# Performance work log

Measured on AMD Instinct MI355X. Metric: run time of the kernel, lower is better.

## Reference

```python
import jax, jax.numpy as jnp
import numpy as np

NUM_HEADS = 12
HEAD_SIZE = 64
HIDDEN = NUM_HEADS * HEAD_SIZE  # 768
ONE_SIDED_WINDOW = 256          # attention_window 512 // 2
NEG = -10000.0


def setup_inputs() -> dict:
    key = jax.random.key(0)
    ks = jax.random.split(key, 16)
    B, W, E, H = 1, 2048, 128, HIDDEN
    std = 0.02
    def lin(kw, kb):
        return (jax.random.normal(kw, (H, H), jnp.float32) * std,
                jax.random.normal(kb, (H,), jnp.float32) * std)
    q_w, q_b = lin(ks[0], ks[1])
    k_w, k_b = lin(ks[2], ks[3])
    v_w, v_b = lin(ks[4], ks[5])
    w2e_w, w2e_b = lin(ks[6], ks[7])
    e2w_w, e2w_b = lin(ks[8], ks[9])
    e2e_w, e2e_b = lin(ks[10], ks[11])
    return {
        "word_hidden_states": jax.random.normal(ks[12], (B, W, H), jnp.float32),
        "entity_hidden_states": jax.random.normal(ks[13], (B, E, H), jnp.float32),
        "attention_mask": jnp.zeros((B, 1, 1, W + E), jnp.float32),
        "q_w": q_w, "q_b": q_b, "k_w": k_w, "k_b": k_b, "v_w": v_w, "v_b": v_b,
        "w2e_w": w2e_w, "w2e_b": w2e_b, "e2w_w": e2w_w, "e2w_b": e2w_b,
        "e2e_w": e2e_w, "e2e_b": e2e_b,
    }


def reference(word_hidden_states, entity_hidden_states, attention_mask,
              q_w, q_b, k_w, k_b, v_w, v_b,
              w2e_w, w2e_b, e2w_w, e2w_b, e2e_w, e2e_b):
    B, W, H = word_hidden_states.shape
    E = entity_hidden_states.shape[1]
    S = W + E

    def heads(x):  # [B, L, H] -> [B, nh, L, hd]
        return x.reshape(B, -1, NUM_HEADS, HEAD_SIZE).transpose(0, 2, 1, 3)

    concat = jnp.concatenate([word_hidden_states, entity_hidden_states], axis=1)
    k = heads(concat @ k_w + k_b)          # [B, nh, S, hd]
    v = heads(concat @ v_w + v_b)
    q_w2w = heads(word_hidden_states @ q_w + q_b)
    q_w2e = heads(word_hidden_states @ w2e_w + w2e_b)
    q_e2w = heads(entity_hidden_states @ e2w_w + e2w_b)
    q_e2e = heads(entity_hidden_states @ e2e_w + e2e_b)

    k_word, k_ent = k[:, :, :W], k[:, :, W:]

    # --- w2w: Longformer sliding-window QK^T, then _conversion to a dense
    # [B, nh, W, W] matrix with out-of-band entries set to -10000. ---
    w2w = jnp.einsum('bhid,bhjd->bhij', q_w2w, k_word)  # [B, nh, W, W]
    idx = jnp.arange(W)
    in_band = jnp.abs(idx[:, None] - idx[None, :]) <= ONE_SIDED_WINDOW  # [W, W]
    # diagonal mask: float_mask[j] (-10000 where attention_mask != 0) added
    # within the band (broadcast over heads / query positions)
    mask_words = attention_mask[:, 0, 0, :W]                # [B, W]
    float_mask = jnp.where(mask_words != 0.0, NEG, 0.0)     # [B, W]
    w2w = w2w + float_mask[:, None, None, :]
    # _conversion: out-of-band -> -10000; also exact zeros -> -10000 (source quirk)
    w2w = jnp.where(in_band[None, None] & (w2w != 0.0), w2w, NEG)

    # --- entity-aware dense blocks ---
    w2e = jnp.einsum('bhid,bhjd->bhij', q_w2e, k_ent)    # [B, nh, W, E]
    e2w = jnp.einsum('bhid,bhjd->bhij', q_e2w, k_word)   # [B, nh, E, W]
    e2e = jnp.einsum('bhid,bhjd->bhij', q_e2e, k_ent)    # [B, nh, E, E]

    word_scores = jnp.concatenate([w2w, w2e], axis=3)    # [B, nh, W, S]
    ent_scores = jnp.concatenate([e2w, e2e], axis=3)     # [B, nh, E, S]
    scores = jnp.concatenate([word_scores, ent_scores], axis=2)  # [B, nh, S, S]

    scores = scores / jnp.sqrt(jnp.float32(HEAD_SIZE)) + attention_mask
    probs = jax.nn.softmax(scores, axis=-1)

    ctx = jnp.einsum('bhij,bhjd->bhid', probs, v)        # [B, nh, S, hd]
    ctx = ctx.transpose(0, 2, 1, 3).reshape(B, S, H)
    return ctx[:, :W, :], ctx[:, W:, :]
```

## Files before the change

### kernel.cpp

```cpp
#include <hip/hip_runtime.h>

typedef __bf16 bf16x8 __attribute__((ext_vector_type(8)));
typedef unsigned short u16x8 __attribute__((ext_vector_type(8)));
typedef u16x8 u16x8_a __attribute__((may_alias));
typedef unsigned int u32x2 __attribute__((ext_vector_type(2)));
typedef u32x2 u32x2_a __attribute__((may_alias));
typedef unsigned int u32x4 __attribute__((ext_vector_type(4)));
typedef u32x4 u32x4_a __attribute__((may_alias));
typedef float f32x4 __attribute__((ext_vector_type(4)));
typedef float f32x16 __attribute__((ext_vector_type(16)));

#define LOG2E 1.4426950408889634f
#define NEGV  -10000.0f

__device__ __forceinline__ unsigned int cvtpk(float lo, float hi){
  unsigned int r;
  asm("v_cvt_pk_bf16_f32 %0, %1, %2" : "=v"(r) : "v"(lo), "v"(hi));
  return r;
}
__device__ __forceinline__ bf16x8 ldb(const unsigned short* p){
  return __builtin_bit_cast(bf16x8, *(const u16x8_a*)p);
}
__device__ __forceinline__ bf16x8 mkfrag(unsigned a, unsigned b, unsigned c, unsigned d){
  u32x4 v = {a,b,c,d};
  return __builtin_bit_cast(bf16x8, v);
}
__device__ __forceinline__ void gload16(const unsigned short* g, unsigned short* l){
  __builtin_amdgcn_global_load_lds(
    (const __attribute__((address_space(1))) void*)g,
    (__attribute__((address_space(3))) void*)l, 16, 0, 0);
}

__global__ __launch_bounds__(256) void prep(
    const float* __restrict__ w0, const float* __restrict__ w1,
    const float* __restrict__ w2, const float* __restrict__ w3,
    const float* __restrict__ w4, const float* __restrict__ w5,
    const float* __restrict__ word, const float* __restrict__ ent,
    const float* __restrict__ am,
    unsigned short* __restrict__ outT, unsigned short* __restrict__ Abf,
    float* __restrict__ amT, float* __restrict__ negT)
{
  int z = blockIdx.z, tid = threadIdx.x;
  if (z == 6){
    size_t id = (size_t)blockIdx.y*24 + blockIdx.x;
    size_t e = (id*256 + tid)*8;
    const size_t WE = (size_t)2048*768;
    const float* s = (e < WE) ? (word + e) : (ent + (e - WE));
    float4 a = *(const float4*)s;
    float4 b = *(const float4*)(s+4);
    u32x4 v = {cvtpk(a.x,a.y), cvtpk(a.z,a.w), cvtpk(b.x,b.y), cvtpk(b.z,b.w)};
    *(u32x4_a*)(Abf + e) = v;
    return;
  }
  if (z == 7){
    if (blockIdx.y != 0 || blockIdx.x >= 9) return;
    int j = blockIdx.x*256 + tid;
    if (j < 2176){
      float a = am[j];
      amT[j]  = a * LOG2E;
      negT[j] = (a != 0.f) ? NEGV : 0.f;
    }
    return;
  }
  if (blockIdx.y >= 24) return;
  const float* src;
  switch (z){
    case 0: src = w0; break; case 1: src = w1; break; case 2: src = w2; break;
    case 3: src = w3; break; case 4: src = w4; break; default: src = w5; break;
  }
  unsigned short* dst = outT + (size_t)z * 589824;
  __shared__ float tile[32][33];
  int tx = tid & 31, ty = tid >> 5;
  int x0 = blockIdx.x*32, y0 = blockIdx.y*32;
  #pragma unroll
  for (int i=0;i<32;i+=8) tile[ty+i][tx] = src[(size_t)(y0+ty+i)*768 + x0+tx];
  __syncthreads();
  #pragma unroll
  for (int i=0;i<32;i+=16){
    unsigned int u = cvtpk(tile[tx][ty+i], tile[tx][ty+i+8]);
    dst[(size_t)(x0+ty+i)*768 + y0+tx]   = (unsigned short)u;
    dst[(size_t)(x0+ty+i+8)*768 + y0+tx] = (unsigned short)(u>>16);
  }
}

__global__ __launch_bounds__(256) void gemm_proj(
    const unsigned short* __restrict__ Abf,
    const unsigned short* __restrict__ wT,
    const float* __restrict__ bK, const float* __restrict__ bV,
    const float* __restrict__ bQ, const float* __restrict__ bWE,
    const float* __restrict__ bEW, const float* __restrict__ bEE,
    unsigned short* __restrict__ oK, unsigned short* __restrict__ VbT,
    unsigned short* __restrict__ oQ, unsigned short* __restrict__ oWE,
    unsigned short* __restrict__ oEW, unsigned short* __restrict__ oEE)
{
  int mt = blockIdx.x, ntile = blockIdx.y;
  int g, mg;
  if      (mt < 17){ g=0; mg=mt;    }
  else if (mt < 34){ g=1; mg=mt-17; }
  else if (mt < 50){ g=2; mg=mt-34; }
  else if (mt < 66){ g=3; mg=mt-50; }
  else if (mt < 67){ g=4; mg=0;     }
  else             { g=5; mg=0;     }
  int m0 = mg*128;
  const unsigned short* A = Abf + (size_t)((g>=4 ? 2048 : 0) + m0)*768;
  const unsigned short* B = wT + (size_t)g*589824;
  const float* bias; unsigned short* out;
  switch (g){
    case 0: bias=bK;  out=oK;  break;
    case 1: bias=bV;  out=0;   break;
    case 2: bias=bQ;  out=oQ;  break;
    case 3: bias=bWE; out=oWE; break;
    case 4: bias=bEW; out=oEW; break;
    default:bias=bEE; out=oEE; break;
  }
  int n0 = ntile*128;

  __shared__ __align__(16) unsigned short a_s[128*32];
  __shared__ __align__(16) unsigned short b_s[128*32];

  int tid  = threadIdx.x;
  int w    = tid>>6, lane = tid&63, quad = lane>>4, lr = lane&15;
  int wm   = (w&1)*64, wn = (w>>1)*64;

  f32x4 acc[4][4];
  #pragma unroll
  for (int i=0;i<4;i++) for (int j=0;j<4;j++) for (int r=0;r<4;r++) acc[i][j][r]=0.f;

  int srow = lane>>2;
  int scol = (lane&3)*8;
  const unsigned short* gA0 = A + (size_t)(w*32 + srow)*768 + scol;
  const unsigned short* gA1 = gA0 + (size_t)16*768;
  const unsigned short* gB0 = B + (size_t)(n0 + w*32 + srow)*768 + scol;
  const unsigned short* gB1 = gB0 + (size_t)16*768;
  unsigned short* lA0 = a_s + w*32*32;
  unsigned short* lA1 = lA0 + 16*32;
  unsigned short* lB0 = b_s + w*32*32;
  unsigned short* lB1 = lB0 + 16*32;

  for (int k0=0; k0<768; k0+=32){
    __syncthreads();
    gload16(gA0 + k0, lA0);
    gload16(gA1 + k0, lA1);
    gload16(gB0 + k0, lB0);
    gload16(gB1 + k0, lB1);
    __syncthreads();
    bf16x8 af[4], bfr[4];
    #pragma unroll
    for (int i=0;i<4;i++) af[i]  = ldb(a_s + (wm+i*16+lr)*32 + quad*8);
    #pragma unroll
    for (int j=0;j<4;j++) bfr[j] = ldb(b_s + (wn+j*16+lr)*32 + quad*8);
    #pragma unroll
    for (int i=0;i<4;i++)
      #pragma unroll
      for (int j=0;j<4;j++)
        acc[i][j] = __builtin_amdgcn_mfma_f32_16x16x32_bf16(af[i], bfr[j], acc[i][j], 0,0,0);
  }
  if (g == 1){
    #pragma unroll
    for (int j=0;j<4;j++){
      int col = n0 + wn + j*16 + lr;
      float bb = bias[col];
      #pragma unroll
      for (int i=0;i<4;i++){
        int rowb = m0 + wm + i*16 + quad*4;
        u32x2 uv = {cvtpk(acc[i][j][0]+bb, acc[i][j][1]+bb),
                    cvtpk(acc[i][j][2]+bb, acc[i][j][3]+bb)};
        *(u32x2_a*)(VbT + (size_t)col*2176 + rowb) = uv;
      }
    }
  } else {
    out += (size_t)m0*768;
    #pragma unroll
    for (int j=0;j<4;j++){
      int col = n0 + wn + j*16 + lr;
      float bb = bias[col];
      #pragma unroll
      for (int i=0;i<4;i++){
        int rowb = wm + i*16 + quad*4;
        unsigned int u01 = cvtpk(acc[i][j][0]+bb, acc[i][j][1]+bb);
        unsigned int u23 = cvtpk(acc[i][j][2]+bb, acc[i][j][3]+bb);
        out[(size_t)(rowb+0)*768 + col] = (unsigned short)u01;
        out[(size_t)(rowb+1)*768 + col] = (unsigned short)(u01>>16);
        out[(size_t)(rowb+2)*768 + col] = (unsigned short)u23;
        out[(size_t)(rowb+3)*768 + col] = (unsigned short)(u23>>16);
      }
    }
  }
}

__global__ __launch_bounds__(256) void attn_split(
  const unsigned short* __restrict__ Kb,  const unsigned short* __restrict__ VbT,
  const unsigned short* __restrict__ Qw,  const unsigned short* __restrict__ Qwe,
  const unsigned short* __restrict__ Qew, const unsigned short* __restrict__ Qee,
  const float* __restrict__ amT, const float* __restrict__ negT,
  float* __restrict__ outw, float* __restrict__ pO, float* __restrict__ pML)
{
  int lin = blockIdx.x + 80*blockIdx.y;
  int wid = (lin & 7)*120 + (lin >> 3);
  int bx = wid % 80;
  int h  = wid / 80;

  int tid = threadIdx.x, w = tid>>6, lane = tid&63;
  int l31 = lane & 31, hi = lane >> 5;
  int hi8 = hi*8, hi4 = hi*4;
  bool isword = bx < 64;
  int qrb, eg=0, eq=0;
  const unsigned short *Qa, *Qb;
  if (isword){ qrb = bx*32; Qa=Qw;  Qb=Qwe; }
  else       { int e = bx-64; eg = e>>2; eq = e&3; qrb = eg*32; Qa=Qew; Qb=Qee; }
  int hofs = h*64;

  __shared__ float part[4][64][35];

  float m = -1e30f, l = 0.f;
  f32x16 o0, o1;
  #pragma unroll
  for (int r=0;r<16;r++){ o0[r] = 0.f; o1[r] = 0.f; }

  int lo, b, s1, endT;
  if (isword){
    lo = qrb - 256; if (lo < 0) lo = 0;
    int hiq = qrb + 288; if (hiq > 2048) hiq = 2048;
    b = (hiq - lo) >> 5;
    s1 = w; endT = b + 4;
  } else {
    lo = 0; b = 64;
    s1 = eq*17 + w; endT = eq*17 + 17;
  }
  int e1 = (b < endT) ? b : endT;
  int c2 = s1 + ((e1 - s1 + 3) & ~3);
  int iq = qrb + l31;

#define BODY(J0, K0, K1, K2, K3, BAND) do { \
    int jb = (J0); \
    float4 aT0 = *(const float4*)(amT + jb + hi4); \
    float4 aT1 = *(const float4*)(amT + jb + 8  + hi4); \
    float4 aT2 = *(const float4*)(amT + jb + 16 + hi4); \
    float4 aT3 = *(const float4*)(amT + jb + 24 + hi4); \
    f32x16 s; \
    _Pragma("unroll") \
    for (int r=0;r<16;r++) s[r] = 0.f; \
    __builtin_amdgcn_s_setprio(1); \
    s = __builtin_amdgcn_mfma_f32_32x32x16_bf16(K0, qf0, s, 0,0,0); \
    s = __builtin_amdgcn_mfma_f32_32x32x16_bf16(K1, qf1, s, 0,0,0); \
    s = __builtin_amdgcn_mfma_f32_32x32x16_bf16(K2, qf2, s, 0,0,0); \
    s = __builtin_amdgcn_mfma_f32_32x32x16_bf16(K3, qf3, s, 0,0,0); \
    __builtin_amdgcn_s_setprio(0); \
    const unsigned short* vp = VbT + (size_t)(hofs + l31)*2176 + jb + hi8; \
    bf16x8 va00 = ldb(vp),           va01 = ldb(vp + 16); \
    bf16x8 va10 = ldb(vp + 32*2176), va11 = ldb(vp + 32*2176 + 16); \
    float sc[16]; \
    if (BAND){ \
      float4 nT0 = *(const float4*)(negT + jb + hi4); \
      float4 nT1 = *(const float4*)(negT + jb + 8  + hi4); \
      float4 nT2 = *(const float4*)(negT + jb + 16 + hi4); \
      float4 nT3 = *(const float4*)(negT + jb + 24 + hi4); \
      int djb = iq + 256 - (jb + hi4); \
      _Pragma("unroll") \
      for (int e=0;e<4;e++){ \
        { float sv = s[e]    + nT0[e]; \
          bool ok = ((unsigned)(djb - e)      <= 512u) && (sv != 0.f); \
          sc[e]    = (ok ? sv : NEGV) * (LOG2E*0.125f) + aT0[e]; } \
        { float sv = s[4+e]  + nT1[e]; \
          bool ok = ((unsigned)(djb - 8 - e)  <= 512u) && (sv != 0.f); \
          sc[4+e]  = (ok ? sv : NEGV) * (LOG2E*0.125f) + aT1[e]; } \
        { float sv = s[8+e]  + nT2[e]; \
          bool ok = ((unsigned)(djb - 16 - e) <= 512u) && (sv != 0.f); \
          sc[8+e]  = (ok ? sv : NEGV) * (LOG2E*0.125f) + aT2[e]; } \
        { float sv = s[12+e] + nT3[e]; \
          bool ok = ((unsigned)(djb - 24 - e) <= 512u) && (sv != 0.f); \
          sc[12+e] = (ok ? sv : NEGV) * (LOG2E*0.125f) + aT3[e]; } \
      } \
    } else { \
      _Pragma("unroll") \
      for (int e=0;e<4;e++){ \
        sc[e]    = s[e]    * (LOG2E*0.125f) + aT0[e]; \
        sc[4+e]  = s[4+e]  * (LOG2E*0.125f) + aT1[e]; \
        sc[8+e]  = s[8+e]  * (LOG2E*0.125f) + aT2[e]; \
        sc[12+e] = s[12+e] * (LOG2E*0.125f) + aT3[e]; \
      } \
    } \
    float mx = sc[0]; \
    _Pragma("unroll") \
    for (int r=1;r<16;r++) mx = fmaxf(mx, sc[r]); \
    mx = fmaxf(mx, __shfl_xor(mx, 32)); \
    float mn; \
    if (__all(mx <= m)){ \
      mn = m; \
    } else { \
      mn = fmaxf(m, mx); \
      float alpha = exp2f(m - mn); \
      m = mn; \
      l *= alpha; \
      _Pragma("unroll") \
      for (int r=0;r<16;r++){ o0[r] *= alpha; o1[r] *= alpha; } \
    } \
    float p[16]; \
    _Pragma("unroll") \
    for (int r=0;r<16;r++) p[r] = exp2f(sc[r]-mn); \
    float rs = ((p[0]+p[1])+(p[2]+p[3])) + ((p[4]+p[5])+(p[6]+p[7])) \
             + ((p[8]+p[9])+(p[10]+p[11])) + ((p[12]+p[13])+(p[14]+p[15])); \
    rs += __shfl_xor(rs, 32); \
    l += rs; \
    unsigned pk0 = cvtpk(p[0], p[1]),  pk1 = cvtpk(p[2], p[3]); \
    unsigned pk2 = cvtpk(p[4], p[5]),  pk3 = cvtpk(p[6], p[7]); \
    unsigned pk4 = cvtpk(p[8], p[9]),  pk5 = cvtpk(p[10], p[11]); \
    unsigned pk6 = cvtpk(p[12], p[13]),pk7 = cvtpk(p[14], p[15]); \
    bool hib = hi != 0; \
    unsigned t0 = hib ? pk0 : pk2; \
    unsigned t1 = hib ? pk1 : pk3; \
    unsigned t2 = hib ? pk4 : pk6; \
    unsigned t3 = hib ? pk5 : pk7; \
    unsigned r0 = (unsigned)__shfl_xor((int)t0, 32); \
    unsigned r1 = (unsigned)__shfl_xor((int)t1, 32); \
    unsigned r2 = (unsigned)__shfl_xor((int)t2, 32); \
    unsigned r3 = (unsigned)__shfl_xor((int)t3, 32); \
    bf16x8 pf1 = hib ? mkfrag(r0, r1, pk2, pk3) : mkfrag(pk0, pk1, r0, r1); \
    bf16x8 pf2 = hib ? mkfrag(r2, r3, pk6, pk7) : mkfrag(pk4, pk5, r2, r3); \
    __builtin_amdgcn_s_setprio(1); \
    o0 = __builtin_amdgcn_mfma_f32_32x32x16_bf16(va00, pf1, o0, 0,0,0); \
    o0 = __builtin_amdgcn_mfma_f32_32x32x16_bf16(va01, pf2, o0, 0,0,0); \
    o1 = __builtin_amdgcn_mfma_f32_32x32x16_bf16(va10, pf1, o1, 0,0,0); \
    o1 = __builtin_amdgcn_mfma_f32_32x32x16_bf16(va11, pf2, o1, 0,0,0); \
    __builtin_amdgcn_s_setprio(0); \
  } while(0)

#define LOADK(K0, K1, K2, K3, J0) do { \
    const unsigned short* kp_ = Kb + (size_t)((J0)+l31)*768 + hofs + hi8; \
    K0 = ldb(kp_); K1 = ldb(kp_+16); K2 = ldb(kp_+32); K3 = ldb(kp_+48); \
  } while(0)

  {
    const unsigned short* qr = Qa + (size_t)(qrb+l31)*768 + hofs + hi8;
    bf16x8 qf0 = ldb(qr), qf1 = ldb(qr+16), qf2 = ldb(qr+32), qf3 = ldb(qr+48);
    bool band = isword;
    bf16x8 kA0,kA1,kA2,kA3, kB0,kB1,kB2,kB3;
    int c = s1;
    LOADK(kA0,kA1,kA2,kA3, lo + c*32);
    while (true){
      int cn = c + 4;
      bool mb = cn < e1;
      if (mb) LOADK(kB0,kB1,kB2,kB3, lo + cn*32);
      BODY(lo + c*32, kA0,kA1,kA2,kA3, band);
      if (!mb) break;
      int cnn = cn + 4;
      bool ma = cnn < e1;
      if (ma) LOADK(kA0,kA1,kA2,kA3, lo + cnn*32);
      BODY(lo + cn*32, kB0,kB1,kB2,kB3, band);
      if (!ma) break;
      c = cnn;
    }
  }
  if (c2 < endT){
    const unsigned short* qr = Qb + (size_t)(qrb+l31)*768 + hofs + hi8;
    bf16x8 qf0 = ldb(qr), qf1 = ldb(qr+16), qf2 = ldb(qr+32), qf3 = ldb(qr+48);
    int j2base = 2048 + (c2 - b)*32;
    bf16x8 kC0,kC1,kC2,kC3;
    LOADK(kC0,kC1,kC2,kC3, j2base);
    BODY(j2base, kC0,kC1,kC2,kC3, false);
  }
#undef BODY
#undef LOADK

  {
    float* my = &part[w][lane][0];
    my[0] = m; my[1] = l;
    #pragma unroll
    for (int r=0;r<16;r++){ my[2+r] = o0[r]; my[18+r] = o1[r]; }
  }
  __syncthreads();

  float mm[4], ll[4], e4[4];
  #pragma unroll
  for (int p=0;p<4;p++){ mm[p] = part[p][lane][0]; ll[p] = part[p][lane][1]; }
  float M = fmaxf(fmaxf(mm[0],mm[1]), fmaxf(mm[2],mm[3]));
  #pragma unroll
  for (int p=0;p<4;p++) e4[p] = exp2f(mm[p]-M);
  float L = ll[0]*e4[0] + ll[1]*e4[1] + ll[2]*e4[2] + ll[3]*e4[3];

  float mo0[4], mo1[4];
  #pragma unroll
  for (int k=0;k<4;k++){
    float a0 = 0.f, a1 = 0.f;
    #pragma unroll
    for (int p=0;p<4;p++){
      a0 += part[p][lane][2  + w*4 + k] * e4[p];
      a1 += part[p][lane][18 + w*4 + k] * e4[p];
    }
    mo0[k] = a0; mo1[k] = a1;
  }

  if (isword){
    float rinv = 1.f / L;
    float4 s0 = {mo0[0]*rinv, mo0[1]*rinv, mo0[2]*rinv, mo0[3]*rinv};
    float4 s1v = {mo1[0]*rinv, mo1[1]*rinv, mo1[2]*rinv, mo1[3]*rinv};
    float* ob = outw + (size_t)(qrb+l31)*768 + hofs + w*8 + hi4;
    *(float4*)(ob)      = s0;
    *(float4*)(ob + 32) = s1v;
  } else {
    int idx = (eg*4 + eq)*12 + h;
    float* po = pO + (size_t)idx*2048 + l31*64 + w*8 + hi4;
    float4 s0 = {mo0[0], mo0[1], mo0[2], mo0[3]};
    float4 s1v = {mo1[0], mo1[1], mo1[2], mo1[3]};
    *(float4*)(po)      = s0;
    *(float4*)(po + 32) = s1v;
    if (w == 0 && lane < 32){
      float* pml = pML + (size_t)idx*64;
      pml[lane*2]     = M;
      pml[lane*2 + 1] = L;
    }
  }
}

__global__ __launch_bounds__(256) void merge_ent(
    const float* __restrict__ pO, const float* __restrict__ pML,
    float* __restrict__ oute)
{
  int b = blockIdx.x;
  int eg = b/12, h = b%12;
  int tid = threadIdx.x;
  int row = tid>>3, cg = (tid&7)*8;
  float mq[4], lq[4];
  #pragma unroll
  for (int q=0;q<4;q++){
    int idx = (eg*4 + q)*12 + h;
    mq[q] = pML[(size_t)idx*64 + row*2];
    lq[q] = pML[(size_t)idx*64 + row*2 + 1];
  }
  float M = fmaxf(fmaxf(mq[0],mq[1]), fmaxf(mq[2],mq[3]));
  float L = 0.f, eqv[4];
  #pragma unroll
  for (int q=0;q<4;q++){ eqv[q] = exp2f(mq[q]-M); L += lq[q]*eqv[q]; }
  float rl = 1.f/L;
  float4 a0 = {0,0,0,0}, a1 = {0,0,0,0};
  #pragma unroll
  for (int q=0;q<4;q++){
    int idx = (eg*4 + q)*12 + h;
    const float* src = pO + (size_t)idx*2048 + row*64 + cg;
    float4 x = *(const float4*)(src);
    float4 y = *(const float4*)(src + 4);
    a0.x += x.x*eqv[q]; a0.y += x.y*eqv[q]; a0.z += x.z*eqv[q]; a0.w += x.w*eqv[q];
    a1.x += y.x*eqv[q]; a1.y += y.y*eqv[q]; a1.z += y.z*eqv[q]; a1.w += y.w*eqv[q];
  }
  a0.x*=rl; a0.y*=rl; a0.z*=rl; a0.w*=rl;
  a1.x*=rl; a1.y*=rl; a1.z*=rl; a1.w*=rl;
  float* dst = oute + (size_t)(eg*32+row)*768 + h*64 + cg;
  *(float4*)(dst)   = a0;
  *(float4*)(dst+4) = a1;
}

extern "C" void kernel_launch(void* const* d_in, const int* in_sizes, int n_in,
                              void* d_out, int out_size, void* d_ws, size_t ws_size,
                              hipStream_t stream) {
  const float* word  = (const float*)d_in[0];
  const float* ent   = (const float*)d_in[1];
  const float* am    = (const float*)d_in[2];
  const float* q_w   = (const float*)d_in[3];
  const float* q_b   = (const float*)d_in[4];
  const float* k_w   = (const float*)d_in[5];
  const float* k_b   = (const float*)d_in[6];
  const float* v_w   = (const float*)d_in[7];
  const float* v_b   = (const float*)d_in[8];
  const float* w2e_w = (const float*)d_in[9];
  const float* w2e_b = (const float*)d_in[10];
  const float* e2w_w = (const float*)d_in[11];
  const float* e2w_b = (const float*)d_in[12];
  const float* e2e_w = (const float*)d_in[13];
  const float* e2e_b = (const float*)d_in[14];

  unsigned short* ws  = (unsigned short*)d_ws;
  unsigned short* wT  = ws;
  unsigned short* Kb  = wT  + (size_t)6*589824;
  unsigned short* Tb  = Kb  + (size_t)2176*768;
  unsigned short* Qw  = Tb  + (size_t)2176*768;
  unsigned short* Qwe = Qw  + (size_t)2048*768;
  unsigned short* Qew = Qwe + (size_t)2048*768;
  unsigned short* Qee = Qew + (size_t)128*768;
  unsigned short* VbT = Qee + (size_t)128*768;
  unsigned short* Abf = VbT + (size_t)768*2176;

  float* amT  = (float*)Tb;
  float* negT = amT + 2176;

  float* pO  = (float*)wT;
  float* pML = pO + (size_t)192*2048;

  float* outw = (float*)d_out;
  float* oute = outw + (size_t)2048*768;

  hipLaunchKernelGGL(prep, dim3(24,34,8), dim3(256), 0, stream,
                     k_w, v_w, q_w, w2e_w, e2w_w, e2e_w, word, ent, am,
                     wT, Abf, amT, negT);
  hipLaunchKernelGGL(gemm_proj, dim3(68,6), dim3(256), 0, stream,
                     Abf, wT, k_b, v_b, q_b, w2e_b, e2w_b, e2e_b,
                     Kb, VbT, Qw, Qwe, Qew, Qee);
  hipLaunchKernelGGL(attn_split, dim3(80,12), dim3(256), 0, stream,
                     Kb, VbT, Qw, Qwe, Qew, Qee, amT, negT, outw, pO, pML);
  hipLaunchKernelGGL(merge_ent, dim3(48), dim3(256), 0, stream,
                     pO, pML, oute);
}
```

Measured before the change: 151.3 us.

## Process two key tiles per iteration with interleaved MFMAs and lazy max rescale

The main attention loop now handles two 32-key tiles per iteration. Their QK^T MFMAs are interleaved, the online-softmax max update is shared across both tiles, and the PV MFMAs are issued back to back, which should expose more instruction-level parallelism and halve the per-tile reduction and shuffle overhead. The old explicit K-register double-buffer prefetch is removed in favour of loading both tiles at the top of each iteration. The rescale condition is relaxed to skip rescaling unless the new max exceeds the running max by more than 8 (in log2 units), which cuts branchy rescale work but risks larger exp values. The change also raises register pressure.

```diff
diff --git a/kernel.cpp b/kernel.cpp
--- a/kernel.cpp
+++ b/kernel.cpp
@@ -231,61 +231,85 @@
   int c2 = s1 + ((e1 - s1 + 3) & ~3);
   int iq = qrb + l31;
 
-#define BODY(J0, K0, K1, K2, K3, BAND) do { \
+#define SCORES(SC, SS, JB, BAND) do { \
+    float4 aT0_ = *(const float4*)(amT + (JB) + hi4); \
+    float4 aT1_ = *(const float4*)(amT + (JB) + 8  + hi4); \
+    float4 aT2_ = *(const float4*)(amT + (JB) + 16 + hi4); \
+    float4 aT3_ = *(const float4*)(amT + (JB) + 24 + hi4); \
+    if (BAND){ \
+      float4 nT0_ = *(const float4*)(negT + (JB) + hi4); \
+      float4 nT1_ = *(const float4*)(negT + (JB) + 8  + hi4); \
+      float4 nT2_ = *(const float4*)(negT + (JB) + 16 + hi4); \
+      float4 nT3_ = *(const float4*)(negT + (JB) + 24 + hi4); \
+      int djb_ = iq + 256 - ((JB) + hi4); \
+      _Pragma("unroll") \
+      for (int e=0;e<4;e++){ \
+        { float sv = (SS)[e]    + nT0_[e]; \
+          bool ok = ((unsigned)(djb_ - e)      <= 512u) && (sv != 0.f); \
+          (SC)[e]    = (ok ? sv : NEGV) * (LOG2E*0.125f) + aT0_[e]; } \
+        { float sv = (SS)[4+e]  + nT1_[e]; \
+          bool ok = ((unsigned)(djb_ - 8 - e)  <= 512u) && (sv != 0.f); \
+          (SC)[4+e]  = (ok ? sv : NEGV) * (LOG2E*0.125f) + aT1_[e]; } \
+        { float sv = (SS)[8+e]  + nT2_[e]; \
+          bool ok = ((unsigned)(djb_ - 16 - e) <= 512u) && (sv != 0.f); \
+          (SC)[8+e]  = (ok ? sv : NEGV) * (LOG2E*0.125f) + aT2_[e]; } \
+        { float sv = (SS)[12+e] + nT3_[e]; \
+          bool ok = ((unsigned)(djb_ - 24 - e) <= 512u) && (sv != 0.f); \
+          (SC)[12+e] = (ok ? sv : NEGV) * (LOG2E*0.125f) + aT3_[e]; } \
+      } \
+    } else { \
+      _Pragma("unroll") \
+      for (int e=0;e<4;e++){ \
+        (SC)[e]    = (SS)[e]    * (LOG2E*0.125f) + aT0_[e]; \
+        (SC)[4+e]  = (SS)[4+e]  * (LOG2E*0.125f) + aT1_[e]; \
+        (SC)[8+e]  = (SS)[8+e]  * (LOG2E*0.125f) + aT2_[e]; \
+        (SC)[12+e] = (SS)[12+e] * (LOG2E*0.125f) + aT3_[e]; \
+      } \
+    } \
+  } while(0)
+
+#define PACKP(PF1, PF2, P) do { \
+    unsigned pk0_ = cvtpk((P)[0], (P)[1]),  pk1_ = cvtpk((P)[2], (P)[3]); \
+    unsigned pk2_ = cvtpk((P)[4], (P)[5]),  pk3_ = cvtpk((P)[6], (P)[7]); \
+    unsigned pk4_ = cvtpk((P)[8], (P)[9]),  pk5_ = cvtpk((P)[10], (P)[11]); \
+    unsigned pk6_ = cvtpk((P)[12], (P)[13]),pk7_ = cvtpk((P)[14], (P)[15]); \
+    bool hib_ = hi != 0; \
+    unsigned t0_ = hib_ ? pk0_ : pk2_; \
+    unsigned t1_ = hib_ ? pk1_ : pk3_; \
+    unsigned t2_ = hib_ ? pk4_ : pk6_; \
+    unsigned t3_ = hib_ ? pk5_ : pk7_; \
+    unsigned r0_ = (unsigned)__shfl_xor((int)t0_, 32); \
+    unsigned r1_ = (unsigned)__shfl_xor((int)t1_, 32); \
+    unsigned r2_ = (unsigned)__shfl_xor((int)t2_, 32); \
+    unsigned r3_ = (unsigned)__shfl_xor((int)t3_, 32); \
+    PF1 = hib_ ? mkfrag(r0_, r1_, pk2_, pk3_) : mkfrag(pk0_, pk1_, r0_, r1_); \
+    PF2 = hib_ ? mkfrag(r2_, r3_, pk6_, pk7_) : mkfrag(pk4_, pk5_, r2_, r3_); \
+  } while(0)
+
+#define BODY(J0, BAND) do { \
     int jb = (J0); \
-    float4 aT0 = *(const float4*)(amT + jb + hi4); \
-    float4 aT1 = *(const float4*)(amT + jb + 8  + hi4); \
-    float4 aT2 = *(const float4*)(amT + jb + 16 + hi4); \
-    float4 aT3 = *(const float4*)(amT + jb + 24 + hi4); \
+    const unsigned short* kp_ = Kb + (size_t)(jb+l31)*768 + hofs + hi8; \
+    bf16x8 k0_ = ldb(kp_), k1_ = ldb(kp_+16), k2_ = ldb(kp_+32), k3_ = ldb(kp_+48); \
     f32x16 s; \
     _Pragma("unroll") \
     for (int r=0;r<16;r++) s[r] = 0.f; \
     __builtin_amdgcn_s_setprio(1); \
-    s = __builtin_amdgcn_mfma_f32_32x32x16_bf16(K0, qf0, s, 0,0,0); \
-    s = __builtin_amdgcn_mfma_f32_32x32x16_bf16(K1, qf1, s, 0,0,0); \
-    s = __builtin_amdgcn_mfma_f32_32x32x16_bf16(K2, qf2, s, 0,0,0); \
-    s = __builtin_amdgcn_mfma_f32_32x32x16_bf16(K3, qf3, s, 0,0,0); \
+    s = __builtin_amdgcn_mfma_f32_32x32x16_bf16(k0_, qf0, s, 0,0,0); \
+    s = __builtin_amdgcn_mfma_f32_32x32x16_bf16(k1_, qf1, s, 0,0,0); \
+    s = __builtin_amdgcn_mfma_f32_32x32x16_bf16(k2_, qf2, s, 0,0,0); \
+    s = __builtin_amdgcn_mfma_f32_32x32x16_bf16(k3_, qf3, s, 0,0,0); \
     __builtin_amdgcn_s_setprio(0); \
-    const unsigned short* vp = VbT + (size_t)(hofs + l31)*2176 + jb + hi8; \
-    bf16x8 va00 = ldb(vp),           va01 = ldb(vp + 16); \
-    bf16x8 va10 = ldb(vp + 32*2176), va11 = ldb(vp + 32*2176 + 16); \
+    const unsigned short* vp_ = VbT + (size_t)(hofs + l31)*2176 + jb + hi8; \
+    bf16x8 va00_ = ldb(vp_),           va01_ = ldb(vp_ + 16); \
+    bf16x8 va10_ = ldb(vp_ + 32*2176), va11_ = ldb(vp_ + 32*2176 + 16); \
     float sc[16]; \
-    if (BAND){ \
-      float4 nT0 = *(const float4*)(negT + jb + hi4); \
-      float4 nT1 = *(const float4*)(negT + jb + 8  + hi4); \
-      float4 nT2 = *(const float4*)(negT + jb + 16 + hi4); \
-      float4 nT3 = *(const float4*)(negT + jb + 24 + hi4); \
-      int djb = iq + 256 - (jb + hi4); \
-      _Pragma("unroll") \
-      for (int e=0;e<4;e++){ \
-        { float sv = s[e]    + nT0[e]; \
-          bool ok = ((unsigned)(djb - e)      <= 512u) && (sv != 0.f); \
-          sc[e]    = (ok ? sv : NEGV) * (LOG2E*0.125f) + aT0[e]; } \
-        { float sv = s[4+e]  + nT1[e]; \
-          bool ok = ((unsigned)(djb - 8 - e)  <= 512u) && (sv != 0.f); \
-          sc[4+e]  = (ok ? sv : NEGV) * (LOG2E*0.125f) + aT1[e]; } \
-        { float sv = s[8+e]  + nT2[e]; \
-          bool ok = ((unsigned)(djb - 16 - e) <= 512u) && (sv != 0.f); \
-          sc[8+e]  = (ok ? sv : NEGV) * (LOG2E*0.125f) + aT2[e]; } \
-        { float sv = s[12+e] + nT3[e]; \
-          bool ok = ((unsigned)(djb - 24 - e) <= 512u) && (sv != 0.f); \
-          sc[12+e] = (ok ? sv : NEGV) * (LOG2E*0.125f) + aT3[e]; } \
-      } \
-    } else { \
-      _Pragma("unroll") \
-      for (int e=0;e<4;e++){ \
-        sc[e]    = s[e]    * (LOG2E*0.125f) + aT0[e]; \
-        sc[4+e]  = s[4+e]  * (LOG2E*0.125f) + aT1[e]; \
-        sc[8+e]  = s[8+e]  * (LOG2E*0.125f) + aT2[e]; \
-        sc[12+e] = s[12+e] * (LOG2E*0.125f) + aT3[e]; \
-      } \
-    } \
+    SCORES(sc, s, jb, BAND); \
     float mx = sc[0]; \
     _Pragma("unroll") \
     for (int r=1;r<16;r++) mx = fmaxf(mx, sc[r]); \
     mx = fmaxf(mx, __shfl_xor(mx, 32)); \
     float mn; \
-    if (__all(mx <= m)){ \
+    if (__all(mx <= m + 8.0f)){ \
       mn = m; \
     } else { \
       mn = fmaxf(m, mx); \
@@ -302,65 +326,103 @@
              + ((p[8]+p[9])+(p[10]+p[11])) + ((p[12]+p[13])+(p[14]+p[15])); \
     rs += __shfl_xor(rs, 32); \
     l += rs; \
-    unsigned pk0 = cvtpk(p[0], p[1]),  pk1 = cvtpk(p[2], p[3]); \
-    unsigned pk2 = cvtpk(p[4], p[5]),  pk3 = cvtpk(p[6], p[7]); \
-    unsigned pk4 = cvtpk(p[8], p[9]),  pk5 = cvtpk(p[10], p[11]); \
-    unsigned pk6 = cvtpk(p[12], p[13]),pk7 = cvtpk(p[14], p[15]); \
-    bool hib = hi != 0; \
-    unsigned t0 = hib ? pk0 : pk2; \
-    unsigned t1 = hib ? pk1 : pk3; \
-    unsigned t2 = hib ? pk4 : pk6; \
-    unsigned t3 = hib ? pk5 : pk7; \
-    unsigned r0 = (unsigned)__shfl_xor((int)t0, 32); \
-    unsigned r1 = (unsigned)__shfl_xor((int)t1, 32); \
-    unsigned r2 = (unsigned)__shfl_xor((int)t2, 32); \
-    unsigned r3 = (unsigned)__shfl_xor((int)t3, 32); \
-    bf16x8 pf1 = hib ? mkfrag(r0, r1, pk2, pk3) : mkfrag(pk0, pk1, r0, r1); \
-    bf16x8 pf2 = hib ? mkfrag(r2, r3, pk6, pk7) : mkfrag(pk4, pk5, r2, r3); \
+    bf16x8 pf1, pf2; \
+    PACKP(pf1, pf2, p); \
     __builtin_amdgcn_s_setprio(1); \
-    o0 = __builtin_amdgcn_mfma_f32_32x32x16_bf16(va00, pf1, o0, 0,0,0); \
-    o0 = __builtin_amdgcn_mfma_f32_32x32x16_bf16(va01, pf2, o0, 0,0,0); \
-    o1 = __builtin_amdgcn_mfma_f32_32x32x16_bf16(va10, pf1, o1, 0,0,0); \
-    o1 = __builtin_amdgcn_mfma_f32_32x32x16_bf16(va11, pf2, o1, 0,0,0); \
+    o0 = __builtin_amdgcn_mfma_f32_32x32x16_bf16(va00_, pf1, o0, 0,0,0); \
+    o0 = __builtin_amdgcn_mfma_f32_32x32x16_bf16(va01_, pf2, o0, 0,0,0); \
+    o1 = __builtin_amdgcn_mfma_f32_32x32x16_bf16(va10_, pf1, o1, 0,0,0); \
+    o1 = __builtin_amdgcn_mfma_f32_32x32x16_bf16(va11_, pf2, o1, 0,0,0); \
     __builtin_amdgcn_s_setprio(0); \
   } while(0)
 
-#define LOADK(K0, K1, K2, K3, J0) do { \
-    const unsigned short* kp_ = Kb + (size_t)((J0)+l31)*768 + hofs + hi8; \
-    K0 = ldb(kp_); K1 = ldb(kp_+16); K2 = ldb(kp_+32); K3 = ldb(kp_+48); \
+#define PBODY(JA, JC, BAND) do { \
+    int ja = (JA), jc = (JC); \
+    const unsigned short* kpa_ = Kb + (size_t)(ja+l31)*768 + hofs + hi8; \
+    bf16x8 kA0_ = ldb(kpa_), kA1_ = ldb(kpa_+16), kA2_ = ldb(kpa_+32), kA3_ = ldb(kpa_+48); \
+    const unsigned short* kpc_ = Kb + (size_t)(jc+l31)*768 + hofs + hi8; \
+    bf16x8 kC0_ = ldb(kpc_), kC1_ = ldb(kpc_+16), kC2_ = ldb(kpc_+32), kC3_ = ldb(kpc_+48); \
+    f32x16 sA, sC; \
+    _Pragma("unroll") \
+    for (int r=0;r<16;r++){ sA[r] = 0.f; sC[r] = 0.f; } \
+    __builtin_amdgcn_s_setprio(1); \
+    sA = __builtin_amdgcn_mfma_f32_32x32x16_bf16(kA0_, qf0, sA, 0,0,0); \
+    sC = __builtin_amdgcn_mfma_f32_32x32x16_bf16(kC0_, qf0, sC, 0,0,0); \
+    sA = __builtin_amdgcn_mfma_f32_32x32x16_bf16(kA1_, qf1, sA, 0,0,0); \
+    sC = __builtin_amdgcn_mfma_f32_32x32x16_bf16(kC1_, qf1, sC, 0,0,0); \
+    sA = __builtin_amdgcn_mfma_f32_32x32x16_bf16(kA2_, qf2, sA, 0,0,0); \
+    sC = __builtin_amdgcn_mfma_f32_32x32x16_bf16(kC2_, qf2, sC, 0,0,0); \
+    sA = __builtin_amdgcn_mfma_f32_32x32x16_bf16(kA3_, qf3, sA, 0,0,0); \
+    sC = __builtin_amdgcn_mfma_f32_32x32x16_bf16(kC3_, qf3, sC, 0,0,0); \
+    __builtin_amdgcn_s_setprio(0); \
+    const unsigned short* vpa_ = VbT + (size_t)(hofs + l31)*2176 + ja + hi8; \
+    bf16x8 vA00_ = ldb(vpa_),           vA01_ = ldb(vpa_ + 16); \
+    bf16x8 vA10_ = ldb(vpa_ + 32*2176), vA11_ = ldb(vpa_ + 32*2176 + 16); \
+    const unsigned short* vpc_ = VbT + (size_t)(hofs + l31)*2176 + jc + hi8; \
+    bf16x8 vC00_ = ldb(vpc_),           vC01_ = ldb(vpc_ + 16); \
+    bf16x8 vC10_ = ldb(vpc_ + 32*2176), vC11_ = ldb(vpc_ + 32*2176 + 16); \
+    float scA[16], scC[16]; \
+    SCORES(scA, sA, ja, BAND); \
+    SCORES(scC, sC, jc, BAND); \
+    float mx = fmaxf(scA[0], scC[0]); \
+    _Pragma("unroll") \
+    for (int r=1;r<16;r++) mx = fmaxf(mx, fmaxf(scA[r], scC[r])); \
+    mx = fmaxf(mx, __shfl_xor(mx, 32)); \
+    float mn; \
+    if (__all(mx <= m + 8.0f)){ \
+      mn = m; \
+    } else { \
+      mn = fmaxf(m, mx); \
+      float alpha = exp2f(m - mn); \
+      m = mn; \
+      l *= alpha; \
+      _Pragma("unroll") \
+      for (int r=0;r<16;r++){ o0[r] *= alpha; o1[r] *= alpha; } \
+    } \
+    float pA[16], pC[16]; \
+    _Pragma("unroll") \
+    for (int r=0;r<16;r++){ pA[r] = exp2f(scA[r]-mn); pC[r] = exp2f(scC[r]-mn); } \
+    float rs = (((pA[0]+pA[1])+(pA[2]+pA[3])) + ((pA[4]+pA[5])+(pA[6]+pA[7]))) \
+             + (((pA[8]+pA[9])+(pA[10]+pA[11])) + ((pA[12]+pA[13])+(pA[14]+pA[15]))) \
+             + (((pC[0]+pC[1])+(pC[2]+pC[3])) + ((pC[4]+pC[5])+(pC[6]+pC[7]))) \
+             + (((pC[8]+pC[9])+(pC[10]+pC[11])) + ((pC[12]+pC[13])+(pC[14]+pC[15]))); \
+    rs += __shfl_xor(rs, 32); \
+    l += rs; \
+    bf16x8 pf1, pf2, pf3, pf4; \
+    PACKP(pf1, pf2, pA); \
+    PACKP(pf3, pf4, pC); \
+    __builtin_amdgcn_s_setprio(1); \
+    o0 = __builtin_amdgcn_mfma_f32_32x32x16_bf16(vA00_, pf1, o0, 0,0,0); \
+    o1 = __builtin_amdgcn_mfma_f32_32x32x16_bf16(vA10_, pf1, o1, 0,0,0); \
+    o0 = __builtin_amdgcn_mfma_f32_32x32x16_bf16(vA01_, pf2, o0, 0,0,0); \
+    o1 = __builtin_amdgcn_mfma_f32_32x32x16_bf16(vA11_, pf2, o1, 0,0,0); \
+    o0 = __builtin_amdgcn_mfma_f32_32x32x16_bf16(vC00_, pf3, o0, 0,0,0); \
+    o1 = __builtin_amdgcn_mfma_f32_32x32x16_bf16(vC10_, pf3, o1, 0,0,0); \
+    o0 = __builtin_amdgcn_mfma_f32_32x32x16_bf16(vC01_, pf4, o0, 0,0,0); \
+    o1 = __builtin_amdgcn_mfma_f32_32x32x16_bf16(vC11_, pf4, o1, 0,0,0); \
+    __builtin_amdgcn_s_setprio(0); \
   } while(0)
 
   {
     const unsigned short* qr = Qa + (size_t)(qrb+l31)*768 + hofs + hi8;
     bf16x8 qf0 = ldb(qr), qf1 = ldb(qr+16), qf2 = ldb(qr+32), qf3 = ldb(qr+48);
     bool band = isword;
-    bf16x8 kA0,kA1,kA2,kA3, kB0,kB1,kB2,kB3;
     int c = s1;
-    LOADK(kA0,kA1,kA2,kA3, lo + c*32);
-    while (true){
-      int cn = c + 4;
-      bool mb = cn < e1;
-      if (mb) LOADK(kB0,kB1,kB2,kB3, lo + cn*32);
-      BODY(lo + c*32, kA0,kA1,kA2,kA3, band);
-      if (!mb) break;
-      int cnn = cn + 4;
-      bool ma = cnn < e1;
-      if (ma) LOADK(kA0,kA1,kA2,kA3, lo + cnn*32);
-      BODY(lo + cn*32, kB0,kB1,kB2,kB3, band);
-      if (!ma) break;
-      c = cnn;
-    }
+    for (; c + 4 < e1; c += 8)
+      PBODY(lo + c*32, lo + (c+4)*32, band);
+    if (c < e1)
+      BODY(lo + c*32, band);
   }
   if (c2 < endT){
     const unsigned short* qr = Qb + (size_t)(qrb+l31)*768 + hofs + hi8;
     bf16x8 qf0 = ldb(qr), qf1 = ldb(qr+16), qf2 = ldb(qr+32), qf3 = ldb(qr+48);
     int j2base = 2048 + (c2 - b)*32;
-    bf16x8 kC0,kC1,kC2,kC3;
-    LOADK(kC0,kC1,kC2,kC3, j2base);
-    BODY(j2base, kC0,kC1,kC2,kC3, false);
+    BODY(j2base, false);
   }
 #undef BODY
-#undef LOADK
+#undef PBODY
+#undef SCORES
+#undef PACKP
 
   {
     float* my = &part[w][lane][0];
```

Measured after the change: 164.7 us. 1.09x slower.
